# Performance work log

Measured on AMD Instinct MI355X. Metric: run time of the kernel, lower is better.

The kernel has to match this reference:

```python
import jax, jax.numpy as jnp
from jax import lax
import numpy as np

B, Q, T, C = 64, 900, 100, 92
W_CLASS, W_BBOX, W_GIOU = 1.0, 1.0, 1.0


def to_corners(b):
    cx, cy, w, h = b[..., 0], b[..., 1], b[..., 2], b[..., 3]
    return jnp.stack([cx - 0.5 * w, cy - 0.5 * h, cx + 0.5 * w, cy + 0.5 * h], axis=-1)


def generalized_iou(b1, b2):
    # b1 [Q,4], b2 [T,4] in corner format -> pairwise GIoU [Q,T]
    a1 = (b1[:, 2] - b1[:, 0]) * (b1[:, 3] - b1[:, 1])
    a2 = (b2[:, 2] - b2[:, 0]) * (b2[:, 3] - b2[:, 1])
    lt = jnp.maximum(b1[:, None, :2], b2[None, :, :2])
    rb = jnp.minimum(b1[:, None, 2:], b2[None, :, 2:])
    wh = jnp.clip(rb - lt, 0.0)
    inter = wh[..., 0] * wh[..., 1]
    union = a1[:, None] + a2[None, :] - inter
    iou = inter / union
    lt_e = jnp.minimum(b1[:, None, :2], b2[None, :, :2])
    rb_e = jnp.maximum(b1[:, None, 2:], b2[None, :, 2:])
    wh_e = jnp.clip(rb_e - lt_e, 0.0)
    area_e = wh_e[..., 0] * wh_e[..., 1]
    return iou - (area_e - union) / area_e


def cost_matrix(logits, pred_bbox, tgt_labels, tgt_bbox):
    conf = jax.nn.softmax(logits, axis=-1)                                  # [B,Q,C]
    cost_class = -jax.vmap(lambda c, l: c[:, l])(conf, tgt_labels)          # [B,Q,T]
    cost_bbox = jnp.sum(jnp.abs(pred_bbox[:, :, None, :] - tgt_bbox[:, None, :, :]), axis=-1)
    cost_giou = -jax.vmap(generalized_iou)(to_corners(pred_bbox), to_corners(tgt_bbox))
    return W_BBOX * cost_bbox + W_CLASS * cost_class + W_GIOU * cost_giou   # [B,Q,T]


def solve_lsa(cost):
    # Jonker-Volgenant shortest-augmenting-path optimal assignment.
    # cost [n, m] with n <= m; assigns every row to a distinct column.
    n, m = cost.shape
    INF = jnp.asarray(1e9, cost.dtype)

    def assign_row(i, carry):
        u, v, p = carry        # u [n+1], v [m+1] potentials; p [m+1]: row assigned to col (0=free)
        p = p.at[0].set(i + 1)
        minv0 = jnp.full(m + 1, INF, cost.dtype)
        used0 = jnp.zeros(m + 1, bool)
        way0 = jnp.zeros(m + 1, jnp.int32)

        def cond(s):
            j0, u, v, p, minv, used, way = s
            return p[j0] != 0

        def body(s):
            j0, u, v, p, minv, used, way = s
            used = used.at[j0].set(True)
            i0 = p[j0]
            cur = cost[i0 - 1] - u[i0] - v[1:]          # reduced costs over cols 1..m
            cur = jnp.where(used[1:], INF, cur)
            better = cur < minv[1:]
            minv = minv.at[1:].set(jnp.where(better, cur, minv[1:]))
            way = way.at[1:].set(jnp.where(better, j0, way[1:]))
            masked = jnp.where(used[1:], INF, minv[1:])
            j1 = jnp.argmin(masked).astype(jnp.int32) + 1
            delta = masked[j1 - 1]
            u = u.at[p].add(jnp.where(used, delta, jnp.zeros((), cost.dtype)))
            v = v - jnp.where(used, delta, jnp.zeros((), cost.dtype))
            minv = minv - jnp.where(used, jnp.zeros((), cost.dtype), delta)
            return j1, u, v, p, minv, used, way

        j0, u, v, p, _, _, way = lax.while_loop(
            cond, body, (jnp.int32(0), u, v, p, minv0, used0, way0))

        def aug_cond(s):
            jj, p = s
            return jj != 0

        def aug_body(s):
            jj, p = s
            j1 = way[jj]
            p = p.at[jj].set(p[j1])
            return j1, p

        _, p = lax.while_loop(aug_cond, aug_body, (j0, p))
        return u, v, p

    u0 = jnp.zeros(n + 1, cost.dtype)
    v0 = jnp.zeros(m + 1, cost.dtype)
    p0 = jnp.zeros(m + 1, jnp.int32)
    _, _, p = lax.fori_loop(0, n, assign_row, (u0, v0, p0))
    # column (0-based) assigned to each row i
    q = jnp.argmax(p[1:, None] == (jnp.arange(n, dtype=jnp.int32) + 1)[None, :], axis=0)
    order = jnp.argsort(q)
    return q[order].astype(jnp.int32), order.astype(jnp.int32)


def setup_inputs() -> dict:
    key = jax.random.key(0)
    k1, k2, k3, k4 = jax.random.split(key, 4)
    return {
        'logits': jax.random.normal(k1, (B, Q, C), jnp.float32),
        'pred_bbox': jax.random.uniform(k2, (B, Q, 4), jnp.float32),
        'tgt_labels': jax.random.randint(k3, (B, T), 0, C, jnp.int32),
        'tgt_bbox': jax.random.uniform(k4, (B, T, 4), jnp.float32),
    }


def reference(logits, pred_bbox, tgt_labels, tgt_bbox):
    cost = cost_matrix(logits, pred_bbox, tgt_labels, tgt_bbox)   # [B,Q,T]
    # scipy solves the [Q,T] problem (Q > T): transpose so rows (targets) <= cols (queries).
    row_ind, col_ind = jax.vmap(lambda c: solve_lsa(c.T))(cost)
    # row_ind: query indices (ascending), col_ind: matched target indices, per image.
    return cost, row_ind, col_ind
```

## Files before the change

kernel.cpp:

```cpp
#include <hip/hip_runtime.h>
#include <cmath>

#define Bq 64
#define Qn 900
#define Tn 100
#define Cn 92
#define INFN 1e9f
#define QT 32
#define NQT 29

__device__ inline unsigned fkey(float x) {
    unsigned u = __float_as_uint(x);
    return (u & 0x80000000u) ? ~u : (u | 0x80000000u);
}
__device__ inline float unfkey(unsigned k) {
    unsigned u = (k & 0x80000000u) ? (k & 0x7FFFFFFFu) : ~k;
    return __uint_as_float(u);
}

__device__ inline unsigned wave_min_u32(unsigned x) {
    unsigned t;
#define DPPSTEP(ctrl)                                                          \
    t = (unsigned)__builtin_amdgcn_update_dpp((int)0xFFFFFFFF, (int)x, ctrl,   \
                                              0xF, 0xF, false);                \
    x = (t < x) ? t : x;
    DPPSTEP(0x111)
    DPPSTEP(0x112)
    DPPSTEP(0x114)
    DPPSTEP(0x118)
    DPPSTEP(0x142)
    DPPSTEP(0x143)
#undef DPPSTEP
    return (unsigned)__builtin_amdgcn_readlane((int)x, 63);
}

__global__ __launch_bounds__(256) void cost_fused_kernel(
        const float* __restrict__ logits,
        const float* __restrict__ pred_bbox,
        const int*   __restrict__ tgt_labels,
        const float* __restrict__ tgt_bbox,
        float* __restrict__ cost,
        float* __restrict__ costT,
        unsigned long long* __restrict__ tilemin)
{
    const int b   = blockIdx.y;
    const int q0  = blockIdx.x * QT;
    const int nq  = (q0 + QT <= Qn) ? QT : (Qn - q0);
    const int tid = threadIdx.x;

    __shared__ float prob[QT * Cn];
    __shared__ float pb_s[QT][4];
    __shared__ float tb_s[Tn][4];
    __shared__ int   lab_s[Tn];
    __shared__ float ctile[QT][Tn + 1];

    {
        const float4* src4 = (const float4*)(logits + ((size_t)b * Qn + q0) * Cn);
        float4* dst4 = (float4*)prob;
        const int n4 = nq * Cn / 4;
        for (int i = tid; i < n4; i += 256) dst4[i] = src4[i];
    }
    if (tid < nq)
        *(float4*)pb_s[tid] = *(const float4*)(pred_bbox + ((size_t)b * Qn + q0 + tid) * 4);
    if (tid < Tn) {
        *(float4*)tb_s[tid] = *(const float4*)(tgt_bbox + ((size_t)b * Tn + tid) * 4);
        lab_s[tid] = tgt_labels[b * Tn + tid];
    }
    __syncthreads();

    const int g = tid >> 3, l8 = tid & 7;
    if (g < nq) {
        float mx = -3.0e38f;
        for (int c = l8; c < Cn; c += 8) mx = fmaxf(mx, prob[g * Cn + c]);
        mx = fmaxf(mx, __shfl_xor(mx, 1));
        mx = fmaxf(mx, __shfl_xor(mx, 2));
        mx = fmaxf(mx, __shfl_xor(mx, 4));
        float s = 0.0f;
        for (int c = l8; c < Cn; c += 8) {
            float e = expf(prob[g * Cn + c] - mx);
            prob[g * Cn + c] = e;
            s += e;
        }
        s += __shfl_xor(s, 1);
        s += __shfl_xor(s, 2);
        s += __shfl_xor(s, 4);
        float inv = 1.0f / s;
        for (int c = l8; c < Cn; c += 8) prob[g * Cn + c] *= inv;
    }
    __syncthreads();

    if (g < nq) {
        const float pcx = pb_s[g][0], pcy = pb_s[g][1],
                    pw  = pb_s[g][2], ph  = pb_s[g][3];
        const float px1 = pcx - 0.5f * pw, py1 = pcy - 0.5f * ph;
        const float px2 = pcx + 0.5f * pw, py2 = pcy + 0.5f * ph;
        const float a1  = (px2 - px1) * (py2 - py1);
        const float* probg = prob + g * Cn;

        #pragma unroll
        for (int t = 0; t < 13; ++t) {
            const int tt = l8 + 8 * t;
            if (tt < Tn) {
                float4 tb = *(const float4*)tb_s[tt];
                const float tcx = tb.x, tcy = tb.y, tw = tb.z, th = tb.w;

                float cclass = -probg[lab_s[tt]];
                float cbbox  = fabsf(pcx - tcx) + fabsf(pcy - tcy)
                             + fabsf(pw - tw)  + fabsf(ph - th);

                float tx1 = tcx - 0.5f * tw, ty1 = tcy - 0.5f * th;
                float tx2 = tcx + 0.5f * tw, ty2 = tcy + 0.5f * th;

                float a2 = (tx2 - tx1) * (ty2 - ty1);
                float iw = fmaxf(fminf(px2, tx2) - fmaxf(px1, tx1), 0.0f);
                float ih = fmaxf(fminf(py2, ty2) - fmaxf(py1, ty1), 0.0f);
                float inter = iw * ih;
                float uni = a1 + a2 - inter;
                float iou = inter / uni;
                float ew = fmaxf(fmaxf(px2, tx2) - fminf(px1, tx1), 0.0f);
                float eh = fmaxf(fmaxf(py2, ty2) - fminf(py1, ty1), 0.0f);
                float ae = ew * eh;
                ctile[g][tt] = cbbox + cclass - (iou - (ae - uni) / ae);
            }
        }
    }
    __syncthreads();

    {
        float* cdst = cost + (size_t)b * Qn * Tn + (size_t)q0 * Tn;
        int qq = tid / Tn, tt = tid - qq * Tn;
        const int total = nq * Tn;
        for (int e = tid; e < total; e += 256) {
            cdst[e] = ctile[qq][tt];
            qq += 2; tt += 56;
            if (tt >= Tn) { tt -= Tn; qq += 1; }
        }
    }

    if (costT) {
        float* tdst = costT + (size_t)b * Qn * Tn + q0;
        if (nq == QT) {
            for (int flat = tid; flat < QT * Tn; flat += 256) {
                int r = flat >> 5, c = flat & 31;
                tdst[(size_t)r * Qn + c] = ctile[c][r];
            }
        } else {
            for (int flat = tid; flat < nq * Tn; flat += 256) {
                int r = flat / nq, c = flat - r * nq;
                tdst[(size_t)r * Qn + c] = ctile[c][r];
            }
        }
    }
    if (tilemin && tid < Tn) {
        float bvv = 3.0e38f; int bq = 0;
        for (int q = 0; q < nq; ++q) {
            float x = ctile[q][tid];
            if (x < bvv) { bvv = x; bq = q; }
        }
        tilemin[((size_t)b * NQT + blockIdx.x) * Tn + tid] =
            ((unsigned long long)fkey(bvv) << 32) | (unsigned)(q0 + bq);
    }
}

template<bool TM>
__global__ __launch_bounds__(256) void jv_kernel(
        const float* __restrict__ costT,
        const unsigned long long* __restrict__ tilemin,
        float* __restrict__ out)
{
    const int b    = blockIdx.x;
    const int tid  = threadIdx.x;
    const int lane = tid & 63;
    const int wv   = tid >> 6;

    __shared__ int   p0_lds[1024];
    __shared__ int   way_lds[1024];
    __shared__ float u_lds[Tn + 1];
    __shared__ int   amin_lds[Tn];
    __shared__ unsigned char asg[Tn];
    __shared__ int   freelist[Tn];
    __shared__ int   nfree_s;
    __shared__ int   qarr[Tn];

    for (int j = tid; j < 1024; j += 256) p0_lds[j] = 0;
    if (tid == 0) nfree_s = 0;
    __syncthreads();

    const float* cb = costT + (size_t)b * Qn * Tn;

    if (TM) {
        if (tid < Tn) {
            unsigned long long best = ~0ull;
            for (int t = 0; t < NQT; ++t) {
                unsigned long long v = tilemin[((size_t)b * NQT + t) * Tn + tid];
                if (v < best) best = v;
            }
            u_lds[tid + 1] = unfkey((unsigned)(best >> 32));
            amin_lds[tid]  = (int)(best & 0xFFFFFFFFu);
        }
    } else {
        for (int r = wv; r < Tn; r += 4) {
            float bv = 3.0e38f; int bj = 0x3fffffff;
            #pragma unroll
            for (int k = 0; k < 15; ++k) {
                int c = lane + 64 * k;
                if (c < Qn) {
                    float x = cb[(size_t)r * Qn + c];
                    if (x < bv) { bv = x; bj = c; }
                }
            }
            #pragma unroll
            for (int off = 1; off < 64; off <<= 1) {
                float ov = __shfl_xor(bv, off);
                int   oj = __shfl_xor(bj, off);
                if (ov < bv || (ov == bv && oj < bj)) { bv = ov; bj = oj; }
            }
            if (lane == 0) { u_lds[r + 1] = bv; amin_lds[r] = bj; }
        }
    }
    __syncthreads();

    if (tid < Tn) {
        int j = amin_lds[tid];
        int old = atomicCAS(&p0_lds[j], 0, tid + 1);
        asg[tid] = (old == 0) ? 1 : 0;
    }
    __syncthreads();
    if (tid < Tn && !asg[tid]) {
        int s = atomicAdd(&nfree_s, 1);
        freelist[s] = tid;
    }
    __syncthreads();
    const int nfree = nfree_s;

    if (wv == 0 && nfree > 0) {
        __builtin_amdgcn_s_setprio(1);
        const int cbase = lane << 4;
        float v_r[16], dist_r[16], rc[16];
        int   p_r[16];
        #pragma unroll
        for (int k = 0; k < 16; ++k) v_r[k] = 0.0f;

#define LOADROW(dst, row1)                                                     \
        {                                                                      \
            const float* rp = cb + (size_t)((row1) - 1) * Qn;                  \
            if (cbase + 16 <= Qn) {                                            \
                _Pragma("unroll")                                              \
                for (int w4 = 0; w4 < 4; ++w4) {                               \
                    float4 f = *(const float4*)(rp + cbase + 4 * w4);          \
                    dst[4*w4+0] = f.x; dst[4*w4+1] = f.y;                      \
                    dst[4*w4+2] = f.z; dst[4*w4+3] = f.w;                      \
                }                                                              \
            } else {                                                           \
                _Pragma("unroll")                                              \
                for (int k = 0; k < 16; ++k)                                   \
                    dst[k] = (cbase + k < Qn) ? rp[cbase + k] : 3.0e38f;       \
            }                                                                  \
        }

        #pragma unroll 1
        for (int s = 0; s < nfree; ++s) {
            const int ri = freelist[s];

            {
                const int4* pp = (const int4*)(p0_lds + cbase);
                int4 a = pp[0], bb = pp[1], cc4 = pp[2], dd4 = pp[3];
                p_r[0]=a.x;  p_r[1]=a.y;  p_r[2]=a.z;  p_r[3]=a.w;
                p_r[4]=bb.x; p_r[5]=bb.y; p_r[6]=bb.z; p_r[7]=bb.w;
                p_r[8]=cc4.x; p_r[9]=cc4.y; p_r[10]=cc4.z; p_r[11]=cc4.w;
                p_r[12]=dd4.x; p_r[13]=dd4.y; p_r[14]=dd4.z; p_r[15]=dd4.w;
            }
            #pragma unroll
            for (int k = 0; k < 16; ++k) dist_r[k] = 3.0e38f;
            unsigned um = 0;
            int   i0   = ri + 1;
            float d0   = 0.0f;
            int   jenc = 0;
            int   sink0 = -1;
            float dstar = 0.0f;

            LOADROW(rc, i0);
            float ui0 = u_lds[i0];

            for (int it = 0; it < Tn + 2; ++it) {
                const float sft = d0 - ui0;
                float m[16];
                #pragma unroll
                for (int k = 0; k < 16; ++k) {
                    const int c = cbase + k;
                    const bool excl = (c >= Qn) || ((um >> k) & 1u);
                    float cand = sft + rc[k] - v_r[k];
                    if (!excl && cand < dist_r[k]) {
                        dist_r[k] = cand;
                        way_lds[(k << 6) | lane] = jenc;
                    }
                    m[k] = excl ? 3.0e38f : dist_r[k];
                }
                float a01 = fminf(m[0], m[1]),   a23 = fminf(m[2], m[3]);
                float a45 = fminf(m[4], m[5]),   a67 = fminf(m[6], m[7]);
                float a89 = fminf(m[8], m[9]),   aAB = fminf(m[10], m[11]);
                float aCD = fminf(m[12], m[13]), aEF = fminf(m[14], m[15]);
                float bv = fminf(fminf(fminf(a01, a23), fminf(a45, a67)),
                                 fminf(fminf(a89, aAB), fminf(aCD, aEF)));

                unsigned gk = wave_min_u32(fkey(bv));
                const float delta = unfkey(gk);

                int pk = 0;
                #pragma unroll
                for (int k = 0; k < 16; ++k)
                    if (m[k] == delta) pk = (cbase + k + 1) | (p_r[k] << 12);
                unsigned long long bal = __ballot(pk != 0);
                int src = __ffsll(bal) - 1;
                pk = __shfl(pk, src);
                const int bestj = (pk & 0xFFF) - 1;
                const int bp    = pk >> 12;

                if (bp == 0) { sink0 = bestj; dstar = delta; break; }

                if ((bestj >> 4) == lane) um |= 1u << (bestj & 15);
                LOADROW(rc, bp);
                ui0 = u_lds[bp];
                d0 = delta; jenc = bestj + 1;
            }

            if (lane == 0) u_lds[ri + 1] += dstar;
            #pragma unroll
            for (int k = 0; k < 16; ++k) {
                if ((um >> k) & 1u) {
                    float dd = dstar - dist_r[k];
                    v_r[k] -= dd;
                    u_lds[p_r[k]] += dd;
                }
            }

            if (lane == 0 && sink0 >= 0) {
                int jj = sink0;
                while (true) {
                    int w = way_lds[((jj & 15) << 6) | (jj >> 4)];
                    if (w == 0) { p0_lds[jj] = ri + 1; break; }
                    p0_lds[jj] = p0_lds[w - 1];
                    jj = w - 1;
                }
            }
            __threadfence_block();
        }
        __builtin_amdgcn_s_setprio(0);
#undef LOADROW
    } else if (nfree > 0 && tid >= 64) {
        float acc = 0.0f;
        for (int ofs = (tid - 64) * 16; ofs < Tn * Qn; ofs += 192 * 16)
            acc += cb[ofs];
        asm volatile("" :: "v"(acc));
    }
    __syncthreads();

    for (int c = tid; c < Qn; c += 256) {
        int r = p0_lds[c];
        if (r) qarr[r - 1] = c;
    }
    __syncthreads();

    float* out_row = out + (size_t)Bq * Qn * Tn + (size_t)b * Tn;
    float* out_col = out_row + (size_t)Bq * Tn;
    for (int i = tid; i < Tn; i += 256) {
        int qi = qarr[i];
        int rank = 0;
        for (int jj = 0; jj < Tn; ++jj) rank += (qarr[jj] < qi) ? 1 : 0;
        out_row[rank] = (float)qi;
        out_col[rank] = (float)i;
    }
}

__global__ __launch_bounds__(256) void jv_compat_kernel(
        const float* __restrict__ cost,
        float* __restrict__ out)
{
    const int b    = blockIdx.x;
    const int tid  = threadIdx.x;
    const int lane = tid & 63;
    const int wv   = tid >> 6;
    const bool act = (tid < Qn / 4);

    __shared__ int   p_lds[Qn + 1];
    __shared__ int   way_lds[Qn + 1];
    __shared__ float u_lds[Tn + 1];
    __shared__ int   amin_lds[Tn];
    __shared__ unsigned char asg[Tn];
    __shared__ int   freelist[Tn];
    __shared__ int   nfree_s;
    __shared__ float redv[2][4];
    __shared__ int   redj[2][4];
    __shared__ int   qarr[Tn];

    for (int j = tid; j <= Qn; j += 256) p_lds[j] = 0;
    if (tid == 0) nfree_s = 0;
    __syncthreads();

    const float* cb = cost + (size_t)b * Qn * Tn;

    for (int r = wv; r < Tn; r += 4) {
        float bv = 3.0e38f; int bj = 0x3fffffff;
        #pragma unroll
        for (int k = 0; k < 15; ++k) {
            int c = lane + 64 * k;
            if (c < Qn) {
                float x = cb[(size_t)c * Tn + r];
                if (x < bv) { bv = x; bj = c; }
            }
        }
        #pragma unroll
        for (int off = 1; off < 64; off <<= 1) {
            float ov = __shfl_xor(bv, off);
            int   oj = __shfl_xor(bj, off);
            if (ov < bv || (ov == bv && oj < bj)) { bv = ov; bj = oj; }
        }
        if (lane == 0) { u_lds[r + 1] = bv; amin_lds[r] = bj; }
    }
    __syncthreads();

    if (tid < Tn) {
        int j = amin_lds[tid];
        int old = atomicCAS(&p_lds[j + 1], 0, tid + 1);
        asg[tid] = (old == 0) ? 1 : 0;
    }
    __syncthreads();
    if (tid < Tn && !asg[tid]) {
        int s = atomicAdd(&nfree_s, 1);
        freelist[s] = tid;
    }
    __syncthreads();
    const int nfree = nfree_s;

    const int cbase = 4 * tid;
    float varr[4] = {0.0f, 0.0f, 0.0f, 0.0f};

    for (int s = 0; s < nfree; ++s) {
        const int ri = freelist[s];
        float minv[4] = {INFN, INFN, INFN, INFN};
        unsigned um = 0;
        int i0 = ri + 1, j0 = 0;
        if (tid == 0) p_lds[0] = i0;

        float c0v = 0, c1v = 0, c2v = 0, c3v = 0;
        if (act) {
            const float* cp = cb + (i0 - 1);
            c0v = cp[(size_t)cbase * Tn];       c1v = cp[(size_t)(cbase + 1) * Tn];
            c2v = cp[(size_t)(cbase + 2) * Tn]; c3v = cp[(size_t)(cbase + 3) * Tn];
        }
        float ui0 = u_lds[i0];

        for (int it = 0; it < Tn + 2; ++it) {
            if (j0 > 0 && act) {
                int cc = j0 - 1;
                if ((cc >> 2) == tid) um |= 1u << (cc & 3);
            }
            float bv = 3.0e9f; int bj = 0x3fffffff;
            if (act) {
                float crr[4] = {c0v, c1v, c2v, c3v};
                #pragma unroll
                for (int k = 0; k < 4; ++k) {
                    if (!((um >> k) & 1u)) {
                        float cur = crr[k] - ui0 - varr[k];
                        if (cur < minv[k]) { minv[k] = cur; way_lds[cbase + k + 1] = j0; }
                        if (minv[k] < bv) { bv = minv[k]; bj = cbase + k + 1; }
                    }
                }
            }
            #pragma unroll
            for (int off = 1; off < 64; off <<= 1) {
                float ov = __shfl_xor(bv, off);
                int   oj = __shfl_xor(bj, off);
                if (ov < bv || (ov == bv && oj < bj)) { bv = ov; bj = oj; }
            }
            const int par = it & 1;
            if (lane == 0) { redv[par][wv] = bv; redj[par][wv] = bj; }
            __syncthreads();
            float delta = redv[par][0]; int bestj = redj[par][0];
            #pragma unroll
            for (int w = 1; w < 4; ++w) {
                float ov = redv[par][w]; int oj = redj[par][w];
                if (ov < delta || (ov == delta && oj < bestj)) { delta = ov; bestj = oj; }
            }
            const int bp = p_lds[bestj];

            float ui_n = 0.0f, n0 = 0, n1 = 0, n2 = 0, n3 = 0;
            if (bp != 0) {
                if (act) {
                    const float* cp = cb + (bp - 1);
                    n0 = cp[(size_t)cbase * Tn];       n1 = cp[(size_t)(cbase + 1) * Tn];
                    n2 = cp[(size_t)(cbase + 2) * Tn]; n3 = cp[(size_t)(cbase + 3) * Tn];
                }
                ui_n = u_lds[bp];
            }

            if (tid == 0) u_lds[ri + 1] += delta;
            if (act) {
                #pragma unroll
                for (int k = 0; k < 4; ++k) {
                    if ((um >> k) & 1u) {
                        varr[k] -= delta;
                        u_lds[p_lds[cbase + k + 1]] += delta;
                    } else {
                        minv[k] -= delta;
                    }
                }
            }
            j0 = bestj;
            if (bp == 0) break;
            i0 = bp; ui0 = ui_n;
            c0v = n0; c1v = n1; c2v = n2; c3v = n3;
        }

        if (tid == 0) {
            int jj = j0;
            while (jj != 0) { int j1 = way_lds[jj]; p_lds[jj] = p_lds[j1]; jj = j1; }
        }
        __syncthreads();
    }

    for (int j = tid + 1; j <= Qn; j += 256) {
        int r = p_lds[j];
        if (r) qarr[r - 1] = j - 1;
    }
    __syncthreads();

    float* out_row = out + (size_t)Bq * Qn * Tn + (size_t)b * Tn;
    float* out_col = out_row + (size_t)Bq * Tn;
    for (int i = tid; i < Tn; i += 256) {
        int qi = qarr[i];
        int rank = 0;
        for (int jj = 0; jj < Tn; ++jj) rank += (qarr[jj] < qi) ? 1 : 0;
        out_row[rank] = (float)qi;
        out_col[rank] = (float)i;
    }
}

extern "C" void kernel_launch(void* const* d_in, const int* in_sizes, int n_in,
                              void* d_out, int out_size, void* d_ws, size_t ws_size,
                              hipStream_t stream) {
    const float* logits     = (const float*)d_in[0];
    const float* pred_bbox  = (const float*)d_in[1];
    const int*   tgt_labels = (const int*)d_in[2];
    const float* tgt_bbox   = (const float*)d_in[3];
    float* out = (float*)d_out;

    const size_t needT  = (size_t)Bq * Qn * Tn * sizeof(float);
    const size_t needTM = needT + (size_t)Bq * NQT * Tn * 8 + 4096;

    if (ws_size >= needTM) {
        float* costT = (float*)d_ws;
        unsigned long long* tilemin = (unsigned long long*)((char*)d_ws + needT);
        hipLaunchKernelGGL(cost_fused_kernel, dim3(NQT, Bq), dim3(256), 0, stream,
                           logits, pred_bbox, tgt_labels, tgt_bbox, out, costT, tilemin);
        hipLaunchKernelGGL((jv_kernel<true>), dim3(Bq), dim3(256), 0, stream,
                           costT, tilemin, out);
    } else if (ws_size >= needT) {
        float* costT = (float*)d_ws;
        hipLaunchKernelGGL(cost_fused_kernel, dim3(NQT, Bq), dim3(256), 0, stream,
                           logits, pred_bbox, tgt_labels, tgt_bbox, out, costT,
                           (unsigned long long*)nullptr);
        hipLaunchKernelGGL((jv_kernel<false>), dim3(Bq), dim3(256), 0, stream,
                           costT, (const unsigned long long*)nullptr, out);
    } else {
        hipLaunchKernelGGL(cost_fused_kernel, dim3(NQT, Bq), dim3(256), 0, stream,
                           logits, pred_bbox, tgt_labels, tgt_bbox, out,
                           (float*)nullptr, (unsigned long long*)nullptr);
        hipLaunchKernelGGL(jv_compat_kernel, dim3(Bq), dim3(256), 0, stream,
                           out, out);
    }
}
```

Measured before the change: 94.03 us.

## Fuse cost computation and JV solve into one per-image kernel

Merges the cost-matrix kernel and the JV assignment kernel into a single kernel with one block per image. Each block loops over all 29 query tiles, computing costs, writing both the output and the transposed workspace, and tracking per-target row minima in registers, so the tilemin buffer and the second launch go away. The priority hints and the L2 prefetch warps are also removed. In exchange the cost phase now runs on only 64 blocks instead of 29×64, which sharply cuts parallelism for that compute- and bandwidth-heavy part.

After: 279.8 us. +197.6%, slower.

```diff
diff --git a/kernel.cpp b/kernel.cpp
--- a/kernel.cpp
+++ b/kernel.cpp
@@ -34,145 +34,24 @@
     return (unsigned)__builtin_amdgcn_readlane((int)x, 63);
 }
 
-__global__ __launch_bounds__(256) void cost_fused_kernel(
+__global__ __launch_bounds__(256) void fused_kernel(
         const float* __restrict__ logits,
         const float* __restrict__ pred_bbox,
         const int*   __restrict__ tgt_labels,
         const float* __restrict__ tgt_bbox,
-        float* __restrict__ cost,
-        float* __restrict__ costT,
-        unsigned long long* __restrict__ tilemin)
+        float* __restrict__ out,
+        float* __restrict__ costT)
 {
-    const int b   = blockIdx.y;
-    const int q0  = blockIdx.x * QT;
-    const int nq  = (q0 + QT <= Qn) ? QT : (Qn - q0);
-    const int tid = threadIdx.x;
+    const int b    = blockIdx.x;
+    const int tid  = threadIdx.x;
+    const int lane = tid & 63;
+    const int wv   = tid >> 6;
 
     __shared__ float prob[QT * Cn];
     __shared__ float pb_s[QT][4];
     __shared__ float tb_s[Tn][4];
     __shared__ int   lab_s[Tn];
     __shared__ float ctile[QT][Tn + 1];
-
-    {
-        const float4* src4 = (const float4*)(logits + ((size_t)b * Qn + q0) * Cn);
-        float4* dst4 = (float4*)prob;
-        const int n4 = nq * Cn / 4;
-        for (int i = tid; i < n4; i += 256) dst4[i] = src4[i];
-    }
-    if (tid < nq)
-        *(float4*)pb_s[tid] = *(const float4*)(pred_bbox + ((size_t)b * Qn + q0 + tid) * 4);
-    if (tid < Tn) {
-        *(float4*)tb_s[tid] = *(const float4*)(tgt_bbox + ((size_t)b * Tn + tid) * 4);
-        lab_s[tid] = tgt_labels[b * Tn + tid];
-    }
-    __syncthreads();
-
-    const int g = tid >> 3, l8 = tid & 7;
-    if (g < nq) {
-        float mx = -3.0e38f;
-        for (int c = l8; c < Cn; c += 8) mx = fmaxf(mx, prob[g * Cn + c]);
-        mx = fmaxf(mx, __shfl_xor(mx, 1));
-        mx = fmaxf(mx, __shfl_xor(mx, 2));
-        mx = fmaxf(mx, __shfl_xor(mx, 4));
-        float s = 0.0f;
-        for (int c = l8; c < Cn; c += 8) {
-            float e = expf(prob[g * Cn + c] - mx);
-            prob[g * Cn + c] = e;
-            s += e;
-        }
-        s += __shfl_xor(s, 1);
-        s += __shfl_xor(s, 2);
-        s += __shfl_xor(s, 4);
-        float inv = 1.0f / s;
-        for (int c = l8; c < Cn; c += 8) prob[g * Cn + c] *= inv;
-    }
-    __syncthreads();
-
-    if (g < nq) {
-        const float pcx = pb_s[g][0], pcy = pb_s[g][1],
-                    pw  = pb_s[g][2], ph  = pb_s[g][3];
-        const float px1 = pcx - 0.5f * pw, py1 = pcy - 0.5f * ph;
-        const float px2 = pcx + 0.5f * pw, py2 = pcy + 0.5f * ph;
-        const float a1  = (px2 - px1) * (py2 - py1);
-        const float* probg = prob + g * Cn;
-
-        #pragma unroll
-        for (int t = 0; t < 13; ++t) {
-            const int tt = l8 + 8 * t;
-            if (tt < Tn) {
-                float4 tb = *(const float4*)tb_s[tt];
-                const float tcx = tb.x, tcy = tb.y, tw = tb.z, th = tb.w;
-
-                float cclass = -probg[lab_s[tt]];
-                float cbbox  = fabsf(pcx - tcx) + fabsf(pcy - tcy)
-                             + fabsf(pw - tw)  + fabsf(ph - th);
-
-                float tx1 = tcx - 0.5f * tw, ty1 = tcy - 0.5f * th;
-                float tx2 = tcx + 0.5f * tw, ty2 = tcy + 0.5f * th;
-
-                float a2 = (tx2 - tx1) * (ty2 - ty1);
-                float iw = fmaxf(fminf(px2, tx2) - fmaxf(px1, tx1), 0.0f);
-                float ih = fmaxf(fminf(py2, ty2) - fmaxf(py1, ty1), 0.0f);
-                float inter = iw * ih;
-                float uni = a1 + a2 - inter;
-                float iou = inter / uni;
-                float ew = fmaxf(fmaxf(px2, tx2) - fminf(px1, tx1), 0.0f);
-                float eh = fmaxf(fmaxf(py2, ty2) - fminf(py1, ty1), 0.0f);
-                float ae = ew * eh;
-                ctile[g][tt] = cbbox + cclass - (iou - (ae - uni) / ae);
-            }
-        }
-    }
-    __syncthreads();
-
-    {
-        float* cdst = cost + (size_t)b * Qn * Tn + (size_t)q0 * Tn;
-        int qq = tid / Tn, tt = tid - qq * Tn;
-        const int total = nq * Tn;
-        for (int e = tid; e < total; e += 256) {
-            cdst[e] = ctile[qq][tt];
-            qq += 2; tt += 56;
-            if (tt >= Tn) { tt -= Tn; qq += 1; }
-        }
-    }
-
-    if (costT) {
-        float* tdst = costT + (size_t)b * Qn * Tn + q0;
-        if (nq == QT) {
-            for (int flat = tid; flat < QT * Tn; flat += 256) {
-                int r = flat >> 5, c = flat & 31;
-                tdst[(size_t)r * Qn + c] = ctile[c][r];
-            }
-        } else {
-            for (int flat = tid; flat < nq * Tn; flat += 256) {
-                int r = flat / nq, c = flat - r * nq;
-                tdst[(size_t)r * Qn + c] = ctile[c][r];
-            }
-        }
-    }
-    if (tilemin && tid < Tn) {
-        float bvv = 3.0e38f; int bq = 0;
-        for (int q = 0; q < nq; ++q) {
-            float x = ctile[q][tid];
-            if (x < bvv) { bvv = x; bq = q; }
-        }
-        tilemin[((size_t)b * NQT + blockIdx.x) * Tn + tid] =
-            ((unsigned long long)fkey(bvv) << 32) | (unsigned)(q0 + bq);
-    }
-}
-
-template<bool TM>
-__global__ __launch_bounds__(256) void jv_kernel(
-        const float* __restrict__ costT,
-        const unsigned long long* __restrict__ tilemin,
-        float* __restrict__ out)
-{
-    const int b    = blockIdx.x;
-    const int tid  = threadIdx.x;
-    const int lane = tid & 63;
-    const int wv   = tid >> 6;
-
     __shared__ int   p0_lds[1024];
     __shared__ int   way_lds[1024];
     __shared__ float u_lds[Tn + 1];
@@ -184,40 +63,122 @@
 
     for (int j = tid; j < 1024; j += 256) p0_lds[j] = 0;
     if (tid == 0) nfree_s = 0;
-    __syncthreads();
-
-    const float* cb = costT + (size_t)b * Qn * Tn;
-
-    if (TM) {
+    if (tid < Tn) {
+        *(float4*)tb_s[tid] = *(const float4*)(tgt_bbox + ((size_t)b * Tn + tid) * 4);
+        lab_s[tid] = tgt_labels[b * Tn + tid];
+    }
+
+    float rbv = 3.0e38f; int rbq = 0;
+    const int g = tid >> 3, l8 = tid & 7;
+
+    float* cbw = costT + (size_t)b * Qn * Tn;
+
+    for (int t = 0; t < NQT; ++t) {
+        const int q0 = t * QT;
+        const int nq = (q0 + QT <= Qn) ? QT : (Qn - q0);
+
+        {
+            const float4* src4 = (const float4*)(logits + ((size_t)b * Qn + q0) * Cn);
+            float4* dst4 = (float4*)prob;
+            const int n4 = nq * Cn / 4;
+            for (int i = tid; i < n4; i += 256) dst4[i] = src4[i];
+        }
+        if (tid < nq)
+            *(float4*)pb_s[tid] = *(const float4*)(pred_bbox + ((size_t)b * Qn + q0 + tid) * 4);
+        __syncthreads();
+
+        if (g < nq) {
+            float mx = -3.0e38f;
+            for (int c = l8; c < Cn; c += 8) mx = fmaxf(mx, prob[g * Cn + c]);
+            mx = fmaxf(mx, __shfl_xor(mx, 1));
+            mx = fmaxf(mx, __shfl_xor(mx, 2));
+            mx = fmaxf(mx, __shfl_xor(mx, 4));
+            float s = 0.0f;
+            for (int c = l8; c < Cn; c += 8) {
+                float e = expf(prob[g * Cn + c] - mx);
+                prob[g * Cn + c] = e;
+                s += e;
+            }
+            s += __shfl_xor(s, 1);
+            s += __shfl_xor(s, 2);
+            s += __shfl_xor(s, 4);
+            float inv = 1.0f / s;
+            for (int c = l8; c < Cn; c += 8) prob[g * Cn + c] *= inv;
+        }
+        __syncthreads();
+
+        if (g < nq) {
+            const float pcx = pb_s[g][0], pcy = pb_s[g][1],
+                        pw  = pb_s[g][2], ph  = pb_s[g][3];
+            const float px1 = pcx - 0.5f * pw, py1 = pcy - 0.5f * ph;
+            const float px2 = pcx + 0.5f * pw, py2 = pcy + 0.5f * ph;
+            const float a1  = (px2 - px1) * (py2 - py1);
+            const float* probg = prob + g * Cn;
+
+            #pragma unroll
+            for (int tt8 = 0; tt8 < 13; ++tt8) {
+                const int tt = l8 + 8 * tt8;
+                if (tt < Tn) {
+                    float4 tb = *(const float4*)tb_s[tt];
+                    const float tcx = tb.x, tcy = tb.y, tw = tb.z, th = tb.w;
+
+                    float cclass = -probg[lab_s[tt]];
+                    float cbbox  = fabsf(pcx - tcx) + fabsf(pcy - tcy)
+                                 + fabsf(pw - tw)  + fabsf(ph - th);
+
+                    float tx1 = tcx - 0.5f * tw, ty1 = tcy - 0.5f * th;
+                    float tx2 = tcx + 0.5f * tw, ty2 = tcy + 0.5f * th;
+
+                    float a2 = (tx2 - tx1) * (ty2 - ty1);
+                    float iw = fmaxf(fminf(px2, tx2) - fmaxf(px1, tx1), 0.0f);
+                    float ih = fmaxf(fminf(py2, ty2) - fmaxf(py1, ty1), 0.0f);
+                    float inter = iw * ih;
+                    float uni = a1 + a2 - inter;
+                    float iou = inter / uni;
+                    float ew = fmaxf(fmaxf(px2, tx2) - fminf(px1, tx1), 0.0f);
+                    float eh = fmaxf(fmaxf(py2, ty2) - fminf(py1, ty1), 0.0f);
+                    float ae = ew * eh;
+                    ctile[g][tt] = cbbox + cclass - (iou - (ae - uni) / ae);
+                }
+            }
+        }
+        __syncthreads();
+
+        {
+            float* cdst = out + (size_t)b * Qn * Tn + (size_t)q0 * Tn;
+            int qq = tid / Tn, tt2 = tid - qq * Tn;
+            const int total = nq * Tn;
+            for (int e = tid; e < total; e += 256) {
+                cdst[e] = ctile[qq][tt2];
+                qq += 2; tt2 += 56;
+                if (tt2 >= Tn) { tt2 -= Tn; qq += 1; }
+            }
+        }
+        {
+            float* tdst = cbw + q0;
+            if (nq == QT) {
+                for (int flat = tid; flat < QT * Tn; flat += 256) {
+                    int r = flat >> 5, c = flat & 31;
+                    tdst[(size_t)r * Qn + c] = ctile[c][r];
+                }
+            } else {
+                for (int flat = tid; flat < nq * Tn; flat += 256) {
+                    int r = flat / nq, c = flat - r * nq;
+                    tdst[(size_t)r * Qn + c] = ctile[c][r];
+                }
+            }
+        }
         if (tid < Tn) {
-            unsigned long long best = ~0ull;
-            for (int t = 0; t < NQT; ++t) {
-                unsigned long long v = tilemin[((size_t)b * NQT + t) * Tn + tid];
-                if (v < best) best = v;
-            }
-            u_lds[tid + 1] = unfkey((unsigned)(best >> 32));
-            amin_lds[tid]  = (int)(best & 0xFFFFFFFFu);
-        }
-    } else {
-        for (int r = wv; r < Tn; r += 4) {
-            float bv = 3.0e38f; int bj = 0x3fffffff;
-            #pragma unroll
-            for (int k = 0; k < 15; ++k) {
-                int c = lane + 64 * k;
-                if (c < Qn) {
-                    float x = cb[(size_t)r * Qn + c];
-                    if (x < bv) { bv = x; bj = c; }
-                }
-            }
-            #pragma unroll
-            for (int off = 1; off < 64; off <<= 1) {
-                float ov = __shfl_xor(bv, off);
-                int   oj = __shfl_xor(bj, off);
-                if (ov < bv || (ov == bv && oj < bj)) { bv = ov; bj = oj; }
-            }
-            if (lane == 0) { u_lds[r + 1] = bv; amin_lds[r] = bj; }
-        }
-    }
+            #pragma unroll 4
+            for (int q = 0; q < nq; ++q) {
+                float x = ctile[q][tid];
+                if (x < rbv) { rbv = x; rbq = q0 + q; }
+            }
+        }
+        __syncthreads();
+    }
+
+    if (tid < Tn) { u_lds[tid + 1] = rbv; amin_lds[tid] = rbq; }
     __syncthreads();
 
     if (tid < Tn) {
@@ -233,8 +194,8 @@
     __syncthreads();
     const int nfree = nfree_s;
 
+    const float* cb = cbw;
     if (wv == 0 && nfree > 0) {
-        __builtin_amdgcn_s_setprio(1);
         const int cbase = lane << 4;
         float v_r[16], dist_r[16], rc[16];
         int   p_r[16];
@@ -345,13 +306,7 @@
             }
             __threadfence_block();
         }
-        __builtin_amdgcn_s_setprio(0);
 #undef LOADROW
-    } else if (nfree > 0 && tid >= 64) {
-        float acc = 0.0f;
-        for (int ofs = (tid - 64) * 16; ofs < Tn * Qn; ofs += 192 * 16)
-            acc += cb[ofs];
-        asm volatile("" :: "v"(acc));
     }
     __syncthreads();
 
@@ -369,6 +324,108 @@
         for (int jj = 0; jj < Tn; ++jj) rank += (qarr[jj] < qi) ? 1 : 0;
         out_row[rank] = (float)qi;
         out_col[rank] = (float)i;
+    }
+}
+
+__global__ __launch_bounds__(256) void cost_fused_kernel(
+        const float* __restrict__ logits,
+        const float* __restrict__ pred_bbox,
+        const int*   __restrict__ tgt_labels,
+        const float* __restrict__ tgt_bbox,
+        float* __restrict__ cost)
+{
+    const int b   = blockIdx.y;
+    const int q0  = blockIdx.x * QT;
+    const int nq  = (q0 + QT <= Qn) ? QT : (Qn - q0);
+    const int tid = threadIdx.x;
+
+    __shared__ float prob[QT * Cn];
+    __shared__ float pb_s[QT][4];
+    __shared__ float tb_s[Tn][4];
+    __shared__ int   lab_s[Tn];
+    __shared__ float ctile[QT][Tn + 1];
+
+    {
+        const float4* src4 = (const float4*)(logits + ((size_t)b * Qn + q0) * Cn);
+        float4* dst4 = (float4*)prob;
+        const int n4 = nq * Cn / 4;
+        for (int i = tid; i < n4; i += 256) dst4[i] = src4[i];
+    }
+    if (tid < nq)
+        *(float4*)pb_s[tid] = *(const float4*)(pred_bbox + ((size_t)b * Qn + q0 + tid) * 4);
+    if (tid < Tn) {
+        *(float4*)tb_s[tid] = *(const float4*)(tgt_bbox + ((size_t)b * Tn + tid) * 4);
+        lab_s[tid] = tgt_labels[b * Tn + tid];
+    }
+    __syncthreads();
+
+    const int g = tid >> 3, l8 = tid & 7;
+    if (g < nq) {
+        float mx = -3.0e38f;
+        for (int c = l8; c < Cn; c += 8) mx = fmaxf(mx, prob[g * Cn + c]);
+        mx = fmaxf(mx, __shfl_xor(mx, 1));
+        mx = fmaxf(mx, __shfl_xor(mx, 2));
+        mx = fmaxf(mx, __shfl_xor(mx, 4));
+        float s = 0.0f;
+        for (int c = l8; c < Cn; c += 8) {
+            float e = expf(prob[g * Cn + c] - mx);
+            prob[g * Cn + c] = e;
+            s += e;
+        }
+        s += __shfl_xor(s, 1);
+        s += __shfl_xor(s, 2);
+        s += __shfl_xor(s, 4);
+        float inv = 1.0f / s;
+        for (int c = l8; c < Cn; c += 8) prob[g * Cn + c] *= inv;
+    }
+    __syncthreads();
+
+    if (g < nq) {
+        const float pcx = pb_s[g][0], pcy = pb_s[g][1],
+                    pw  = pb_s[g][2], ph  = pb_s[g][3];
+        const float px1 = pcx - 0.5f * pw, py1 = pcy - 0.5f * ph;
+        const float px2 = pcx + 0.5f * pw, py2 = pcy + 0.5f * ph;
+        const float a1  = (px2 - px1) * (py2 - py1);
+        const float* probg = prob + g * Cn;
+
+        #pragma unroll
+        for (int t = 0; t < 13; ++t) {
+            const int tt = l8 + 8 * t;
+            if (tt < Tn) {
+                float4 tb = *(const float4*)tb_s[tt];
+                const float tcx = tb.x, tcy = tb.y, tw = tb.z, th = tb.w;
+
+                float cclass = -probg[lab_s[tt]];
+                float cbbox  = fabsf(pcx - tcx) + fabsf(pcy - tcy)
+                             + fabsf(pw - tw)  + fabsf(ph - th);
+
+                float tx1 = tcx - 0.5f * tw, ty1 = tcy - 0.5f * th;
+                float tx2 = tcx + 0.5f * tw, ty2 = tcy + 0.5f * th;
+
+                float a2 = (tx2 - tx1) * (ty2 - ty1);
+                float iw = fmaxf(fminf(px2, tx2) - fmaxf(px1, tx1), 0.0f);
+                float ih = fmaxf(fminf(py2, ty2) - fmaxf(py1, ty1), 0.0f);
+                float inter = iw * ih;
+                float uni = a1 + a2 - inter;
+                float iou = inter / uni;
+                float ew = fmaxf(fmaxf(px2, tx2) - fminf(px1, tx1), 0.0f);
+                float eh = fmaxf(fmaxf(py2, ty2) - fminf(py1, ty1), 0.0f);
+                float ae = ew * eh;
+                ctile[g][tt] = cbbox + cclass - (iou - (ae - uni) / ae);
+            }
+        }
+    }
+    __syncthreads();
+
+    {
+        float* cdst = cost + (size_t)b * Qn * Tn + (size_t)q0 * Tn;
+        int qq = tid / Tn, tt = tid - qq * Tn;
+        const int total = nq * Tn;
+        for (int e = tid; e < total; e += 256) {
+            cdst[e] = ctile[qq][tt];
+            qq += 2; tt += 56;
+            if (tt >= Tn) { tt -= Tn; qq += 1; }
+        }
     }
 }
 
@@ -545,27 +602,15 @@
     const float* tgt_bbox   = (const float*)d_in[3];
     float* out = (float*)d_out;
 
-    const size_t needT  = (size_t)Bq * Qn * Tn * sizeof(float);
-    const size_t needTM = needT + (size_t)Bq * NQT * Tn * 8 + 4096;
-
-    if (ws_size >= needTM) {
+    const size_t needT = (size_t)Bq * Qn * Tn * sizeof(float);
+
+    if (ws_size >= needT) {
         float* costT = (float*)d_ws;
-        unsigned long long* tilemin = (unsigned long long*)((char*)d_ws + needT);
-        hipLaunchKernelGGL(cost_fused_kernel, dim3(NQT, Bq), dim3(256), 0, stream,
-                           logits, pred_bbox, tgt_labels, tgt_bbox, out, costT, tilemin);
-        hipLaunchKernelGGL((jv_kernel<true>), dim3(Bq), dim3(256), 0, stream,
-                           costT, tilemin, out);
-    } else if (ws_size >= needT) {
-        float* costT = (float*)d_ws;
-        hipLaunchKernelGGL(cost_fused_kernel, dim3(NQT, Bq), dim3(256), 0, stream,
-                           logits, pred_bbox, tgt_labels, tgt_bbox, out, costT,
-                           (unsigned long long*)nullptr);
-        hipLaunchKernelGGL((jv_kernel<false>), dim3(Bq), dim3(256), 0, stream,
-                           costT, (const unsigned long long*)nullptr, out);
+        hipLaunchKernelGGL(fused_kernel, dim3(Bq), dim3(256), 0, stream,
+                           logits, pred_bbox, tgt_labels, tgt_bbox, out, costT);
     } else {
         hipLaunchKernelGGL(cost_fused_kernel, dim3(NQT, Bq), dim3(256), 0, stream,
-                           logits, pred_bbox, tgt_labels, tgt_bbox, out,
-                           (float*)nullptr, (unsigned long long*)nullptr);
+                           logits, pred_bbox, tgt_labels, tgt_bbox, out);
         hipLaunchKernelGGL(jv_compat_kernel, dim3(Bq), dim3(256), 0, stream,
                            out, out);
     }
```
